# Kernel optimization log

Measured on AMD Instinct MI355X. Metric: run time of the kernel, lower is better.

Reference implementation:

```python
import jax, jax.numpy as jnp
import numpy as np

B, S, D = 4, 1024, 1024
H, HD = 16, 64  # num_heads, head_dim; H*HD == D (qkv_features)
NEG_BIG = -1e10


def setup_inputs() -> dict:
    key = jax.random.key(0)
    ks = jax.random.split(key, 16)
    inp = {
        'inputs_q': jax.random.normal(ks[0], (B, S, D), jnp.float32),
        'inputs_kv': jax.random.normal(ks[1], (B, S, D), jnp.float32),
        'pos_emb_q': jax.random.normal(ks[2], (B, S, D), jnp.float32),
        'pos_emb_k': jax.random.normal(ks[3], (B, S, D), jnp.float32),
        'pos_emb_v': jax.random.normal(ks[4], (B, S, D), jnp.float32),
        'key_padding_mask': jnp.ones((B, S), jnp.float32),
    }
    scale = 1.0 / np.sqrt(D)
    inp['wq'] = jax.random.normal(ks[5], (D, H, HD), jnp.float32) * scale
    inp['bq'] = jnp.zeros((H, HD), jnp.float32)
    inp['wk'] = jax.random.normal(ks[6], (D, H, HD), jnp.float32) * scale
    inp['bk'] = jnp.zeros((H, HD), jnp.float32)
    inp['wv'] = jax.random.normal(ks[7], (D, H, HD), jnp.float32) * scale
    inp['bv'] = jnp.zeros((H, HD), jnp.float32)
    inp['wo'] = jax.random.normal(ks[8], (H, HD, D), jnp.float32) * scale
    inp['bo'] = jnp.zeros((D,), jnp.float32)
    return inp


def reference(inputs_q, inputs_kv, pos_emb_q, pos_emb_k, pos_emb_v,
              key_padding_mask, wq, bq, wk, bk, wv, bv, wo, bo):
    # Add positional embeddings before QKV projections (DETR style).
    q_in = inputs_q + pos_emb_q
    k_in = inputs_kv + pos_emb_k
    v_in = inputs_kv + pos_emb_v
    # DenseGeneral: [b,s,f] x [f,h,d] -> [b,s,h,d]
    q = jnp.einsum('bsf,fhd->bshd', q_in, wq) + bq
    k = jnp.einsum('bsf,fhd->bshd', k_in, wk) + bk
    v = jnp.einsum('bsf,fhd->bshd', v_in, wv) + bv
    # Additive key-padding bias, broadcast to [b,1,1,kv].
    bias = ((1.0 - key_padding_mask) * NEG_BIG)[:, None, None, :]
    q = q / jnp.sqrt(jnp.asarray(HD, q.dtype))
    attn = jnp.einsum('bqhd,bkhd->bhqk', q, k) + bias
    attn = jax.nn.softmax(attn, axis=-1)
    # (train=False: no dropout; identity capture layer is a no-op.)
    x = jnp.einsum('bhqk,bkhd->bqhd', attn, v)
    # Output projection over (heads, head_dim).
    out = jnp.einsum('bqhd,hdf->bqf', x, wo) + bo
    return out
```

## Files before the change

kernel.cpp:

```cpp
#include <hip/hip_runtime.h>
#include <hip/hip_bf16.h>
#include <stdint.h>

typedef __bf16 bf16_t;
typedef __bf16 bf16x8 __attribute__((ext_vector_type(8)));
typedef __bf16 bf16x4v __attribute__((ext_vector_type(4)));
typedef float  f32x4  __attribute__((ext_vector_type(4)));
typedef float  f32x16 __attribute__((ext_vector_type(16)));
typedef unsigned int u32;
typedef u32 u32x4 __attribute__((ext_vector_type(4)));

#define NEG_BIG (-1e10f)

__device__ __forceinline__ void load_lds16(const void* gsrc, void* ldst) {
  __builtin_amdgcn_global_load_lds(
      (__attribute__((address_space(1))) void*)(gsrc),
      (__attribute__((address_space(3))) void*)(ldst), 16, 0, 0);
}

__device__ __forceinline__ u32 cvt_pk_bf16(float lo, float hi) {
  u32 r;
  asm("v_cvt_pk_bf16_f32 %0, %1, %2" : "=v"(r) : "v"(lo), "v"(hi));
  return r;
}

__global__ __launch_bounds__(256) void k_prep_w(
    const float* __restrict__ iq, const float* __restrict__ ikv,
    const float* __restrict__ pq, const float* __restrict__ pk, const float* __restrict__ pv,
    const float* __restrict__ wq, const float* __restrict__ wk,
    const float* __restrict__ wv, const float* __restrict__ wo,
    bf16_t* __restrict__ Xq, bf16_t* __restrict__ Xk, bf16_t* __restrict__ Xv,
    bf16_t* __restrict__ Wt, bf16_t* __restrict__ Wot)
{
  __shared__ float t[64][65];
  if (blockIdx.x < 4096) {
    int i = blockIdx.x * 256 + threadIdx.x;
    float4 a = ((const float4*)iq)[i], b = ((const float4*)ikv)[i];
    float4 eq = ((const float4*)pq)[i], ek = ((const float4*)pk)[i], ev = ((const float4*)pv)[i];
    bf16x4v q, k, v;
    q[0] = (bf16_t)(a.x + eq.x); q[1] = (bf16_t)(a.y + eq.y);
    q[2] = (bf16_t)(a.z + eq.z); q[3] = (bf16_t)(a.w + eq.w);
    k[0] = (bf16_t)(b.x + ek.x); k[1] = (bf16_t)(b.y + ek.y);
    k[2] = (bf16_t)(b.z + ek.z); k[3] = (bf16_t)(b.w + ek.w);
    v[0] = (bf16_t)(b.x + ev.x); v[1] = (bf16_t)(b.y + ev.y);
    v[2] = (bf16_t)(b.z + ev.z); v[3] = (bf16_t)(b.w + ev.w);
    *(bf16x4v*)&Xq[(size_t)i*4] = q;
    *(bf16x4v*)&Xk[(size_t)i*4] = k;
    *(bf16x4v*)&Xv[(size_t)i*4] = v;
  } else {
    int bid = blockIdx.x - 4096;
    int z = bid >> 8, rem = bid & 255;
    const float* src = z==0 ? wq : z==1 ? wk : z==2 ? wv : wo;
    bf16_t*      dst = z < 3 ? (Wt + (size_t)z*(1u<<20)) : Wot;
    int n0 = (rem & 15) << 6, k0 = (rem >> 4) << 6;
    int c = threadIdx.x & 63, rb = threadIdx.x >> 6;
    #pragma unroll
    for (int i = 0; i < 16; ++i) {
      int r = i*4 + rb;
      t[r][c] = src[(size_t)(k0 + r)*1024 + n0 + c];
    }
    __syncthreads();
    #pragma unroll
    for (int i = 0; i < 16; ++i) {
      int r = i*4 + rb;
      dst[(size_t)(n0 + r)*1024 + k0 + c] = (bf16_t)t[c][r];
    }
  }
}

__global__ __launch_bounds__(256, 3) void k_gemm_qkv(
    const bf16_t* __restrict__ Xq, const bf16_t* __restrict__ Xk, const bf16_t* __restrict__ Xv,
    const bf16_t* __restrict__ Wt,
    const float* __restrict__ bq, const float* __restrict__ bk, const float* __restrict__ bv,
    bf16_t* __restrict__ Qo, bf16_t* __restrict__ Ko, bf16_t* __restrict__ Vt)
{
  const int L = blockIdx.x;
  const int w = (L & 7) * 96 + (L >> 3);
  const int bx = w & 7, by = (w >> 3) & 31, bz = w >> 8;
  const int bn = bz * 8 + bx;

  const bf16_t* A = bz==0 ? Xq : bz==1 ? Xk : Xv;
  const float* bias = bz==0 ? bq : bz==1 ? bk : bv;

  __shared__ bf16_t As[128*64];
  __shared__ bf16_t Bs[128*64];

  const int tid = threadIdx.x, lane = tid & 63, wid = tid >> 6;
  const int wm = wid >> 1, wn = wid & 1;
  const int bm0 = by * 128;
  const int bn0g = bn * 128;
  const int g = lane >> 4, c = lane & 15;
  const int sr = lane >> 3, sch = lane & 7;

  f32x4 acc[4][4] = {};

  #define STAGE(kt_)                                                             \
    { _Pragma("unroll")                                                          \
      for (int i = 0; i < 4; ++i) {                                              \
        int r  = wid*32 + i*8 + sr;                                              \
        int ca = sch ^ (r & 7);                                                  \
        load_lds16(A  + (size_t)(bm0  + r)*1024 + (size_t)(kt_)*64 + ca*8,       \
                   &As[(wid*32 + i*8)*64]);                                      \
        load_lds16(Wt + (size_t)(bn0g + r)*1024 + (size_t)(kt_)*64 + ca*8,       \
                   &Bs[(wid*32 + i*8)*64]);                                      \
      } }

  for (int kt = 0; kt < 16; ++kt) {
    STAGE(kt);
    __syncthreads();
    #pragma unroll
    for (int kk = 0; kk < 2; ++kk) {
      bf16x8 af[4], bfr[4];
      #pragma unroll
      for (int m = 0; m < 4; ++m) {
        int row = wm*64 + m*16 + c;
        int ch  = (kk*4 + g) ^ (row & 7);
        af[m] = *(const bf16x8*)&As[row*64 + ch*8];
      }
      #pragma unroll
      for (int n = 0; n < 4; ++n) {
        int row = wn*64 + n*16 + c;
        int ch  = (kk*4 + g) ^ (row & 7);
        bfr[n] = *(const bf16x8*)&Bs[row*64 + ch*8];
      }
      #pragma unroll
      for (int m = 0; m < 4; ++m)
        #pragma unroll
        for (int n = 0; n < 4; ++n)
          acc[m][n] = __builtin_amdgcn_mfma_f32_16x16x32_bf16(af[m], bfr[n], acc[m][n], 0, 0, 0);
    }
    __syncthreads();
  }
  #undef STAGE

  if (bz < 2) {
    bf16_t* C = bz==0 ? Qo : Ko;
    const float scale = bz==0 ? 0.125f : 1.0f;
    #pragma unroll
    for (int n = 0; n < 4; ++n) {
      int col = (bn0g & 1023) + wn*64 + n*16 + c;
      float bn_ = bias[col];
      #pragma unroll
      for (int m = 0; m < 4; ++m) {
        int row0 = bm0 + wm*64 + m*16 + g*4;
        #pragma unroll
        for (int r = 0; r < 4; ++r)
          C[(size_t)(row0 + r)*1024 + col] = (bf16_t)((acc[m][n][r] + bn_) * scale);
      }
    }
  } else {
    #pragma unroll
    for (int n = 0; n < 4; ++n) {
      int colz = (bn0g & 1023) + wn*64 + n*16 + c;
      float bn_ = bias[colz];
      int h = colz >> 6, hd = colz & 63;
      #pragma unroll
      for (int m = 0; m < 4; ++m) {
        int row0 = bm0 + wm*64 + m*16 + g*4;
        int b = row0 >> 10, s0 = row0 & 1023;
        bf16x4v v4;
        #pragma unroll
        for (int r = 0; r < 4; ++r) v4[r] = (bf16_t)(acc[m][n][r] + bn_);
        *(bf16x4v*)&Vt[(size_t)((b*16 + h)*64 + hd)*1024 + s0] = v4;
      }
    }
  }
}

__global__ __launch_bounds__(256, 2) void k_attn2(
    const bf16_t* __restrict__ Qm, const bf16_t* __restrict__ Km,
    const bf16_t* __restrict__ Vt, const float* __restrict__ mask,
    bf16_t* __restrict__ X2)
{
  __shared__ bf16_t Ks[2][64*64];
  __shared__ bf16_t Vs[2][64*64];
  __shared__ float  bias_lds[1024];
  __shared__ float  l_lds[4][32];

  const int qt = blockIdx.x, h = blockIdx.y, b = blockIdx.z;
  const int tid = threadIdx.x, lane = tid & 63, wid = tid >> 6;
  const int lq = lane & 31;
  const int hi = lane >> 5;

  {
    float4 m4 = *(const float4*)&mask[b*1024 + tid*4];
    float4 b4;
    b4.x = (1.0f - m4.x) * NEG_BIG;
    b4.y = (1.0f - m4.y) * NEG_BIG;
    b4.z = (1.0f - m4.z) * NEG_BIG;
    b4.w = (1.0f - m4.w) * NEG_BIG;
    *(float4*)&bias_lds[tid*4] = b4;
  }

  const int q0w = qt*128 + wid*32;
  bf16x8 qf[4];
  #pragma unroll
  for (int kb = 0; kb < 4; ++kb)
    qf[kb] = *(const bf16x8*)&Qm[(size_t)(b*1024 + q0w + lq)*1024 + h*64 + kb*16 + hi*8];

  f32x16 oacc[2] = {};
  float mrow = -1e30f, lsum = 0.f;

  const int sr8 = (lane >> 3);
  const int sc8 = lane & 7;
  #define STAGE(bufi, kv0)                                                        \
    {                                                                             \
      _Pragma("unroll")                                                           \
      for (int cc = 0; cc < 2; ++cc) {                                            \
        int r  = cc*32 + wid*8 + sr8;                                             \
        int ca = sc8 ^ (r & 7);                                                   \
        load_lds16(Km + (size_t)(b*1024 + (kv0) + r)*1024 + h*64 + ca*8,          \
                   &Ks[bufi][(cc*32 + wid*8)*64]);                                \
        load_lds16(Vt + (size_t)((b*16 + h)*64 + r)*1024 + (kv0) + ca*8,          \
                   &Vs[bufi][(cc*32 + wid*8)*64]);                                \
      }                                                                           \
    }

  STAGE(0, 0);
  __syncthreads();

  for (int kt = 0; kt < 16; ++kt) {
    const int buf = kt & 1;
    if (kt < 15) STAGE(buf ^ 1, (kt + 1) * 64);

    f32x16 s[2];
    #pragma unroll
    for (int blk = 0; blk < 2; ++blk) {
      f32x16 acc = {};
      #pragma unroll
      for (int kb = 0; kb < 4; ++kb) {
        int row = blk*32 + lq;
        int ch  = (kb*2 + hi) ^ (row & 7);
        bf16x8 kf = *(const bf16x8*)&Ks[buf][row*64 + ch*8];
        acc = __builtin_amdgcn_mfma_f32_32x32x16_bf16(kf, qf[kb], acc, 0, 0, 0);
      }
      s[blk] = acc;
    }

    #pragma unroll
    for (int blk = 0; blk < 2; ++blk)
      #pragma unroll
      for (int g2 = 0; g2 < 4; ++g2) {
        float4 b4 = *(const float4*)&bias_lds[kt*64 + blk*32 + g2*8 + hi*4];
        s[blk][g2*4+0] += b4.x;
        s[blk][g2*4+1] += b4.y;
        s[blk][g2*4+2] += b4.z;
        s[blk][g2*4+3] += b4.w;
      }

    float pmax = s[0][0];
    #pragma unroll
    for (int blk = 0; blk < 2; ++blk)
      #pragma unroll
      for (int r = 0; r < 16; ++r) pmax = fmaxf(pmax, s[blk][r]);
    pmax = fmaxf(pmax, __shfl_xor(pmax, 32, 64));

    if (!__all(pmax - mrow <= 8.0f)) {
      float mnew = fmaxf(mrow, pmax);
      float sc = __expf(mrow - mnew);
      lsum *= sc;
      #pragma unroll
      for (int nb = 0; nb < 2; ++nb)
        #pragma unroll
        for (int i = 0; i < 16; ++i) oacc[nb][i] *= sc;
      mrow = mnew;
    }

    float rs = 0.f;
    #pragma unroll
    for (int blk = 0; blk < 2; ++blk)
      #pragma unroll
      for (int r = 0; r < 16; ++r) {
        float p = __expf(s[blk][r] - mrow);
        s[blk][r] = p;
        rs += p;
      }
    lsum += rs + __shfl_xor(rs, 32, 64);

    u32 paw[4][4];
    #pragma unroll
    for (int blk = 0; blk < 2; ++blk)
      #pragma unroll
      for (int half = 0; half < 2; ++half) {
        int base = half * 8;
        #pragma unroll
        for (int w2 = 0; w2 < 2; ++w2) {
          u32 x = cvt_pk_bf16(s[blk][base + 2*w2],     s[blk][base + 2*w2 + 1]);
          u32 y = cvt_pk_bf16(s[blk][base + 4 + 2*w2], s[blk][base + 4 + 2*w2 + 1]);
          asm("v_permlane32_swap_b32 %0, %1" : "+v"(x), "+v"(y));
          paw[blk*2 + half][w2]     = x;
          paw[blk*2 + half][w2 + 2] = y;
        }
      }

    #pragma unroll
    for (int ks = 0; ks < 4; ++ks) {
      u32x4 t = { paw[ks][0], paw[ks][1], paw[ks][2], paw[ks][3] };
      bf16x8 pa = __builtin_bit_cast(bf16x8, t);
      #pragma unroll
      for (int nb = 0; nb < 2; ++nb) {
        int row = nb*32 + lq;
        int ch  = (ks*2 + hi) ^ (row & 7);
        bf16x8 vf = *(const bf16x8*)&Vs[buf][row*64 + ch*8];
        oacc[nb] = __builtin_amdgcn_mfma_f32_32x32x16_bf16(pa, vf, oacc[nb], 0, 0, 0);
      }
    }
    __syncthreads();
  }

  l_lds[wid][lq] = lsum;
  __syncthreads();
  #pragma unroll
  for (int g2 = 0; g2 < 4; ++g2)
    #pragma unroll
    for (int j = 0; j < 4; ++j) {
      int reg  = g2*4 + j;
      int qrow = j + 8*g2 + 4*hi;
      float inv = 1.0f / l_lds[wid][qrow];
      #pragma unroll
      for (int nb = 0; nb < 2; ++nb)
        X2[(size_t)(b*1024 + q0w + qrow)*1024 + h*64 + nb*32 + lq] =
            (bf16_t)(oacc[nb][reg] * inv);
    }
  #undef STAGE
}

__global__ __launch_bounds__(256, 3) void k_gemm_out(
    const bf16_t* __restrict__ A, const bf16_t* __restrict__ Bt,
    const float* __restrict__ bo, float* __restrict__ C)
{
  const int L = blockIdx.x;
  const int w = (L & 7) * 32 + (L >> 3);
  const int bx = w & 7, by = w >> 3;

  __shared__ bf16_t As[128*64];
  __shared__ bf16_t Bs[128*64];

  const int tid = threadIdx.x, lane = tid & 63, wid = tid >> 6;
  const int wm = wid >> 1, wn = wid & 1;
  const int bm0 = by * 128, bn0 = bx * 128;
  const int g = lane >> 4, c = lane & 15;
  const int sr = lane >> 3, sch = lane & 7;

  f32x4 acc[4][4] = {};

  #define STAGEO(kt_)                                                            \
    { _Pragma("unroll")                                                          \
      for (int i = 0; i < 4; ++i) {                                              \
        int r  = wid*32 + i*8 + sr;                                              \
        int ca = sch ^ (r & 7);                                                  \
        load_lds16(A  + (size_t)(bm0 + r)*1024 + (size_t)(kt_)*64 + ca*8,        \
                   &As[(wid*32 + i*8)*64]);                                      \
        load_lds16(Bt + (size_t)(bn0 + r)*1024 + (size_t)(kt_)*64 + ca*8,        \
                   &Bs[(wid*32 + i*8)*64]);                                      \
      } }

  for (int kt = 0; kt < 16; ++kt) {
    STAGEO(kt);
    __syncthreads();
    #pragma unroll
    for (int kk = 0; kk < 2; ++kk) {
      bf16x8 af[4], bfr[4];
      #pragma unroll
      for (int m = 0; m < 4; ++m) {
        int row = wm*64 + m*16 + c;
        int ch  = (kk*4 + g) ^ (row & 7);
        af[m] = *(const bf16x8*)&As[row*64 + ch*8];
      }
      #pragma unroll
      for (int n = 0; n < 4; ++n) {
        int row = wn*64 + n*16 + c;
        int ch  = (kk*4 + g) ^ (row & 7);
        bfr[n] = *(const bf16x8*)&Bs[row*64 + ch*8];
      }
      #pragma unroll
      for (int m = 0; m < 4; ++m)
        #pragma unroll
        for (int n = 0; n < 4; ++n)
          acc[m][n] = __builtin_amdgcn_mfma_f32_16x16x32_bf16(af[m], bfr[n], acc[m][n], 0, 0, 0);
    }
    __syncthreads();
  }
  #undef STAGEO

  #pragma unroll
  for (int n = 0; n < 4; ++n) {
    int col = bn0 + wn*64 + n*16 + c;
    float bn_ = bo[col];
    #pragma unroll
    for (int m = 0; m < 4; ++m) {
      int row0 = bm0 + wm*64 + m*16 + g*4;
      #pragma unroll
      for (int r = 0; r < 4; ++r)
        C[(size_t)(row0 + r)*1024 + col] = acc[m][n][r] + bn_;
    }
  }
}

extern "C" void kernel_launch(void* const* d_in, const int* in_sizes, int n_in,
                              void* d_out, int out_size, void* d_ws, size_t ws_size,
                              hipStream_t stream) {
  const float* iq   = (const float*)d_in[0];
  const float* ikv  = (const float*)d_in[1];
  const float* pq   = (const float*)d_in[2];
  const float* pk   = (const float*)d_in[3];
  const float* pv   = (const float*)d_in[4];
  const float* mask = (const float*)d_in[5];
  const float* wq   = (const float*)d_in[6];
  const float* bq   = (const float*)d_in[7];
  const float* wk   = (const float*)d_in[8];
  const float* bk   = (const float*)d_in[9];
  const float* wv   = (const float*)d_in[10];
  const float* bv   = (const float*)d_in[11];
  const float* wo   = (const float*)d_in[12];
  const float* bo   = (const float*)d_in[13];
  float* out = (float*)d_out;

  char* ws = (char*)d_ws;
  bf16_t* Xq  = (bf16_t*)(ws + (size_t)( 0u<<20));
  bf16_t* Xk  = (bf16_t*)(ws + (size_t)( 8u<<20));
  bf16_t* Xv  = (bf16_t*)(ws + (size_t)(16u<<20));
  bf16_t* Wt  = (bf16_t*)(ws + (size_t)(24u<<20));
  bf16_t* Wot = (bf16_t*)(ws + (size_t)(30u<<20));
  bf16_t* Q   = (bf16_t*)(ws + (size_t)(32u<<20));
  bf16_t* K   = (bf16_t*)(ws + (size_t)(40u<<20));
  bf16_t* Vt  = (bf16_t*)(ws + (size_t)(56u<<20));
  bf16_t* X2  = (bf16_t*)(ws + (size_t)(64u<<20));

  k_prep_w<<<5120, 256, 0, stream>>>(iq, ikv, pq, pk, pv, wq, wk, wv, wo,
                                     Xq, Xk, Xv, Wt, Wot);
  k_gemm_qkv<<<768, 256, 0, stream>>>(Xq, Xk, Xv, Wt, bq, bk, bv, Q, K, Vt);
  k_attn2<<<dim3(8,16,4), 256, 0, stream>>>(Q, K, Vt, mask, X2);
  k_gemm_out<<<256, 256, 0, stream>>>(X2, Wot, bo, out);
}
```

Before: 112.1 us.

## Restructure QKV GEMM into 256x256 tiles with double-buffered phased pipeline

Rewrites the QKV projection GEMM to use 512-thread blocks that each compute a 256x256 tile, split into four 128x128 quadrant phases. Global-to-LDS loads for later k-steps are interleaved with MFMA phases, using double-buffered LDS, explicit vmcnt waits and barriers. The goal is to overlap memory traffic with compute and raise data reuse per load. It also raises wave priority around MFMA sections in both the GEMM and the attention kernel. The trade-off is much larger LDS use (128KB) and only 192 blocks, which lowers occupancy and may leave some CUs underused.

```diff
diff --git a/kernel.cpp b/kernel.cpp
--- a/kernel.cpp
+++ b/kernel.cpp
@@ -68,102 +68,128 @@
   }
 }
 
-__global__ __launch_bounds__(256, 3) void k_gemm_qkv(
+__global__ __launch_bounds__(512, 2) void k_gemm_qkv(
     const bf16_t* __restrict__ Xq, const bf16_t* __restrict__ Xk, const bf16_t* __restrict__ Xv,
     const bf16_t* __restrict__ Wt,
     const float* __restrict__ bq, const float* __restrict__ bk, const float* __restrict__ bv,
     bf16_t* __restrict__ Qo, bf16_t* __restrict__ Ko, bf16_t* __restrict__ Vt)
 {
   const int L = blockIdx.x;
-  const int w = (L & 7) * 96 + (L >> 3);
-  const int bx = w & 7, by = (w >> 3) & 31, bz = w >> 8;
-  const int bn = bz * 8 + bx;
-
+  const int w = (L & 7) * 24 + (L >> 3);
+  const int by = w & 15, bn = w >> 4;
+  const int bz = bn >> 2;
   const bf16_t* A = bz==0 ? Xq : bz==1 ? Xk : Xv;
   const float* bias = bz==0 ? bq : bz==1 ? bk : bv;
 
-  __shared__ bf16_t As[128*64];
-  __shared__ bf16_t Bs[128*64];
+  __shared__ bf16_t As[2][2][128*64];
+  __shared__ bf16_t Bs[2][2][128*64];
 
   const int tid = threadIdx.x, lane = tid & 63, wid = tid >> 6;
-  const int wm = wid >> 1, wn = wid & 1;
-  const int bm0 = by * 128;
-  const int bn0g = bn * 128;
+  const int wr = wid >> 2, wc = wid & 3;
+  const int bm0 = by * 256;
+  const int bn0g = bn * 256;
   const int g = lane >> 4, c = lane & 15;
-  const int sr = lane >> 3, sch = lane & 7;
-
-  f32x4 acc[4][4] = {};
-
-  #define STAGE(kt_)                                                             \
-    { _Pragma("unroll")                                                          \
-      for (int i = 0; i < 4; ++i) {                                              \
-        int r  = wid*32 + i*8 + sr;                                              \
-        int ca = sch ^ (r & 7);                                                  \
-        load_lds16(A  + (size_t)(bm0  + r)*1024 + (size_t)(kt_)*64 + ca*8,       \
-                   &As[(wid*32 + i*8)*64]);                                      \
-        load_lds16(Wt + (size_t)(bn0g + r)*1024 + (size_t)(kt_)*64 + ca*8,       \
-                   &Bs[(wid*32 + i*8)*64]);                                      \
-      } }
-
-  for (int kt = 0; kt < 16; ++kt) {
-    STAGE(kt);
-    __syncthreads();
-    #pragma unroll
-    for (int kk = 0; kk < 2; ++kk) {
-      bf16x8 af[4], bfr[4];
-      #pragma unroll
-      for (int m = 0; m < 4; ++m) {
-        int row = wm*64 + m*16 + c;
-        int ch  = (kk*4 + g) ^ (row & 7);
-        af[m] = *(const bf16x8*)&As[row*64 + ch*8];
-      }
-      #pragma unroll
-      for (int n = 0; n < 4; ++n) {
-        int row = wn*64 + n*16 + c;
-        int ch  = (kk*4 + g) ^ (row & 7);
-        bfr[n] = *(const bf16x8*)&Bs[row*64 + ch*8];
-      }
-      #pragma unroll
-      for (int m = 0; m < 4; ++m)
-        #pragma unroll
-        for (int n = 0; n < 4; ++n)
-          acc[m][n] = __builtin_amdgcn_mfma_f32_16x16x32_bf16(af[m], bfr[n], acc[m][n], 0, 0, 0);
-    }
-    __syncthreads();
-  }
-  #undef STAGE
-
+  const int sr = lane >> 3, sc = lane & 7;
+
+  f32x4 acc[2][2][4][2] = {};
+
+  #define STAGE_A(b, h, kt_) { _Pragma("unroll") for (int ld = 0; ld < 2; ++ld) {   \
+      int lr = ld*64 + wid*8 + sr;                                                  \
+      load_lds16(A + (size_t)(bm0 + (h)*128 + lr)*1024 + (size_t)(kt_)*64 + (sc ^ sr)*8, \
+                 &As[b][h][(ld*64 + wid*8)*64]); } }
+  #define STAGE_B(b, h, kt_) { _Pragma("unroll") for (int ld = 0; ld < 2; ++ld) {   \
+      int lr = ld*64 + wid*8 + sr;                                                  \
+      load_lds16(Wt + (size_t)(bn0g + (h)*128 + lr)*1024 + (size_t)(kt_)*64 + (sc ^ sr)*8, \
+                 &Bs[b][h][(ld*64 + wid*8)*64]); } }
+
+  #define PHASE(MH, NH, STAGE_STMT, WAIT_STMT) {                                    \
+    STAGE_STMT;                                                                     \
+    bf16x8 af[4][2], bfv[2][2];                                                     \
+    _Pragma("unroll") for (int m = 0; m < 4; ++m)                                   \
+      _Pragma("unroll") for (int kk = 0; kk < 2; ++kk)                              \
+        af[m][kk] = *(const bf16x8*)&As[buf][MH][(wr*64 + m*16 + c)*64 +            \
+                                                 (((kk)*4 + g) ^ (c & 7))*8];       \
+    _Pragma("unroll") for (int n = 0; n < 2; ++n)                                   \
+      _Pragma("unroll") for (int kk = 0; kk < 2; ++kk)                              \
+        bfv[n][kk] = *(const bf16x8*)&Bs[buf][NH][(wc*32 + n*16 + c)*64 +           \
+                                                  (((kk)*4 + g) ^ (c & 7))*8];      \
+    WAIT_STMT;                                                                      \
+    __builtin_amdgcn_sched_barrier(0);                                              \
+    __builtin_amdgcn_s_barrier();                                                   \
+    __builtin_amdgcn_sched_barrier(0);                                              \
+    __builtin_amdgcn_s_setprio(1);                                                  \
+    _Pragma("unroll") for (int m = 0; m < 4; ++m)                                   \
+      _Pragma("unroll") for (int n = 0; n < 2; ++n)                                 \
+        _Pragma("unroll") for (int kk = 0; kk < 2; ++kk)                            \
+          acc[MH][NH][m][n] = __builtin_amdgcn_mfma_f32_16x16x32_bf16(              \
+              af[m][kk], bfv[n][kk], acc[MH][NH][m][n], 0, 0, 0);                   \
+    __builtin_amdgcn_s_setprio(0);                                                  \
+    __builtin_amdgcn_sched_barrier(0);                                              \
+    __builtin_amdgcn_s_barrier();                                                   \
+    __builtin_amdgcn_sched_barrier(0);                                              \
+  }
+
+  STAGE_A(0, 0, 0); STAGE_B(0, 0, 0); STAGE_B(0, 1, 0); STAGE_A(0, 1, 0);
+  STAGE_A(1, 0, 1); STAGE_B(1, 0, 1);
+  asm volatile("s_waitcnt vmcnt(4)" ::: "memory");
+  __builtin_amdgcn_sched_barrier(0);
+  __builtin_amdgcn_s_barrier();
+  __builtin_amdgcn_sched_barrier(0);
+
+  #pragma unroll 1
+  for (int t = 0; t < 16; ++t) {
+    const int buf = t & 1;
+    PHASE(0, 0, if (t < 15) STAGE_B(buf ^ 1, 1, t + 1), );
+    PHASE(0, 1, if (t < 15) STAGE_A(buf ^ 1, 1, t + 1), );
+    PHASE(1, 0, if (t < 14) STAGE_A(buf, 0, t + 2), );
+    PHASE(1, 1, if (t < 14) STAGE_B(buf, 0, t + 2),
+          if (t < 14)       { asm volatile("s_waitcnt vmcnt(4)" ::: "memory"); }
+          else if (t == 14) { asm volatile("s_waitcnt vmcnt(0)" ::: "memory"); } );
+  }
+  #undef PHASE
+  #undef STAGE_A
+  #undef STAGE_B
+
+  const int bn0loc = (bn & 3) * 256;
   if (bz < 2) {
     bf16_t* C = bz==0 ? Qo : Ko;
     const float scale = bz==0 ? 0.125f : 1.0f;
     #pragma unroll
-    for (int n = 0; n < 4; ++n) {
-      int col = (bn0g & 1023) + wn*64 + n*16 + c;
-      float bn_ = bias[col];
-      #pragma unroll
-      for (int m = 0; m < 4; ++m) {
-        int row0 = bm0 + wm*64 + m*16 + g*4;
+    for (int mh = 0; mh < 2; ++mh)
+      #pragma unroll
+      for (int nh = 0; nh < 2; ++nh)
         #pragma unroll
-        for (int r = 0; r < 4; ++r)
-          C[(size_t)(row0 + r)*1024 + col] = (bf16_t)((acc[m][n][r] + bn_) * scale);
-      }
-    }
+        for (int n = 0; n < 2; ++n) {
+          int col = bn0loc + nh*128 + wc*32 + n*16 + c;
+          float bn_ = bias[col];
+          #pragma unroll
+          for (int m = 0; m < 4; ++m) {
+            int row0 = bm0 + mh*128 + wr*64 + m*16 + g*4;
+            #pragma unroll
+            for (int r = 0; r < 4; ++r)
+              C[(size_t)(row0 + r)*1024 + col] = (bf16_t)((acc[mh][nh][m][n][r] + bn_) * scale);
+          }
+        }
   } else {
     #pragma unroll
-    for (int n = 0; n < 4; ++n) {
-      int colz = (bn0g & 1023) + wn*64 + n*16 + c;
-      float bn_ = bias[colz];
-      int h = colz >> 6, hd = colz & 63;
-      #pragma unroll
-      for (int m = 0; m < 4; ++m) {
-        int row0 = bm0 + wm*64 + m*16 + g*4;
-        int b = row0 >> 10, s0 = row0 & 1023;
-        bf16x4v v4;
+    for (int mh = 0; mh < 2; ++mh)
+      #pragma unroll
+      for (int nh = 0; nh < 2; ++nh)
         #pragma unroll
-        for (int r = 0; r < 4; ++r) v4[r] = (bf16_t)(acc[m][n][r] + bn_);
-        *(bf16x4v*)&Vt[(size_t)((b*16 + h)*64 + hd)*1024 + s0] = v4;
-      }
-    }
+        for (int n = 0; n < 2; ++n) {
+          int colz = bn0loc + nh*128 + wc*32 + n*16 + c;
+          float bn_ = bias[colz];
+          int h = colz >> 6, hd = colz & 63;
+          #pragma unroll
+          for (int m = 0; m < 4; ++m) {
+            int row0 = bm0 + mh*128 + wr*64 + m*16 + g*4;
+            int b = row0 >> 10, s0 = row0 & 1023;
+            bf16x4v v4;
+            #pragma unroll
+            for (int r = 0; r < 4; ++r) v4[r] = (bf16_t)(acc[mh][nh][m][n][r] + bn_);
+            *(bf16x4v*)&Vt[(size_t)((b*16 + h)*64 + hd)*1024 + s0] = v4;
+          }
+        }
   }
 }
 
@@ -224,6 +250,7 @@
     if (kt < 15) STAGE(buf ^ 1, (kt + 1) * 64);
 
     f32x16 s[2];
+    __builtin_amdgcn_s_setprio(1);
     #pragma unroll
     for (int blk = 0; blk < 2; ++blk) {
       f32x16 acc = {};
@@ -236,6 +263,7 @@
       }
       s[blk] = acc;
     }
+    __builtin_amdgcn_s_setprio(0);
 
     #pragma unroll
     for (int blk = 0; blk < 2; ++blk)
@@ -293,6 +321,7 @@
         }
       }
 
+    __builtin_amdgcn_s_setprio(1);
     #pragma unroll
     for (int ks = 0; ks < 4; ++ks) {
       u32x4 t = { paw[ks][0], paw[ks][1], paw[ks][2], paw[ks][3] };
@@ -305,6 +334,7 @@
         oacc[nb] = __builtin_amdgcn_mfma_f32_32x32x16_bf16(pa, vf, oacc[nb], 0, 0, 0);
       }
     }
+    __builtin_amdgcn_s_setprio(0);
     __syncthreads();
   }
 
@@ -429,7 +459,7 @@
 
   k_prep_w<<<5120, 256, 0, stream>>>(iq, ikv, pq, pk, pv, wq, wk, wv, wo,
                                      Xq, Xk, Xv, Wt, Wot);
-  k_gemm_qkv<<<768, 256, 0, stream>>>(Xq, Xk, Xv, Wt, bq, bk, bv, Q, K, Vt);
+  k_gemm_qkv<<<192, 512, 0, stream>>>(Xq, Xk, Xv, Wt, bq, bk, bv, Q, K, Vt);
   k_attn2<<<dim3(8,16,4), 256, 0, stream>>>(Q, K, Vt, mask, X2);
   k_gemm_out<<<256, 256, 0, stream>>>(X2, Wot, bo, out);
 }
```

Measured after the change: 129.5 us. 15.5% more time.

## Load K/V fragments directly from global into registers in attention kernel

Applied to the files above, without the earlier changes.

The attention kernel no longer double-buffers K and V tiles through LDS with async global-to-LDS loads. Each wave now reads its MFMA operand fragments straight from global memory into registers, relying on L2/L1 since the four waves share the same K/V rows. This drops the per-iteration block barrier and the LDS footprint, and final normalization uses a wave shuffle instead of an LDS round trip. s_setprio is added around the MFMA sections. In exchange there is no explicit prefetch, global traffic per wave rises, and the uncoalesced strided reads may add latency.

```diff
diff --git a/kernel.cpp b/kernel.cpp
--- a/kernel.cpp
+++ b/kernel.cpp
@@ -172,10 +172,7 @@
     const bf16_t* __restrict__ Vt, const float* __restrict__ mask,
     bf16_t* __restrict__ X2)
 {
-  __shared__ bf16_t Ks[2][64*64];
-  __shared__ bf16_t Vs[2][64*64];
-  __shared__ float  bias_lds[1024];
-  __shared__ float  l_lds[4][32];
+  __shared__ float bias_lds[1024];
 
   const int qt = blockIdx.x, h = blockIdx.y, b = blockIdx.z;
   const int tid = threadIdx.x, lane = tid & 63, wid = tid >> 6;
@@ -201,47 +198,44 @@
   f32x16 oacc[2] = {};
   float mrow = -1e30f, lsum = 0.f;
 
-  const int sr8 = (lane >> 3);
-  const int sc8 = lane & 7;
-  #define STAGE(bufi, kv0)                                                        \
-    {                                                                             \
-      _Pragma("unroll")                                                           \
-      for (int cc = 0; cc < 2; ++cc) {                                            \
-        int r  = cc*32 + wid*8 + sr8;                                             \
-        int ca = sc8 ^ (r & 7);                                                   \
-        load_lds16(Km + (size_t)(b*1024 + (kv0) + r)*1024 + h*64 + ca*8,          \
-                   &Ks[bufi][(cc*32 + wid*8)*64]);                                \
-        load_lds16(Vt + (size_t)((b*16 + h)*64 + r)*1024 + (kv0) + ca*8,          \
-                   &Vs[bufi][(cc*32 + wid*8)*64]);                                \
-      }                                                                           \
-    }
-
-  STAGE(0, 0);
+  const bf16_t* Kb = Km + (size_t)(b*1024)*1024 + h*64;
+  const bf16_t* Vb = Vt + (size_t)((b*16 + h)*64)*1024;
+
   __syncthreads();
 
   for (int kt = 0; kt < 16; ++kt) {
-    const int buf = kt & 1;
-    if (kt < 15) STAGE(buf ^ 1, (kt + 1) * 64);
+    const int kv0 = kt * 64;
+
+    bf16x8 kf[2][4];
+    #pragma unroll
+    for (int blk = 0; blk < 2; ++blk)
+      #pragma unroll
+      for (int kb = 0; kb < 4; ++kb)
+        kf[blk][kb] = *(const bf16x8*)&Kb[(size_t)(kv0 + blk*32 + lq)*1024 + (kb*2 + hi)*8];
+    bf16x8 vf[4][2];
+    #pragma unroll
+    for (int ks = 0; ks < 4; ++ks)
+      #pragma unroll
+      for (int nb = 0; nb < 2; ++nb)
+        vf[ks][nb] = *(const bf16x8*)&Vb[(size_t)(nb*32 + lq)*1024 + kv0 + (ks*2 + hi)*8];
 
     f32x16 s[2];
+    __builtin_amdgcn_s_setprio(1);
     #pragma unroll
     for (int blk = 0; blk < 2; ++blk) {
       f32x16 acc = {};
       #pragma unroll
-      for (int kb = 0; kb < 4; ++kb) {
-        int row = blk*32 + lq;
-        int ch  = (kb*2 + hi) ^ (row & 7);
-        bf16x8 kf = *(const bf16x8*)&Ks[buf][row*64 + ch*8];
-        acc = __builtin_amdgcn_mfma_f32_32x32x16_bf16(kf, qf[kb], acc, 0, 0, 0);
-      }
+      for (int kb = 0; kb < 4; ++kb)
+        acc = __builtin_amdgcn_mfma_f32_32x32x16_bf16(kf[blk][kb], qf[kb], acc, 0, 0, 0);
       s[blk] = acc;
     }
+    __builtin_amdgcn_s_setprio(0);
 
     #pragma unroll
     for (int blk = 0; blk < 2; ++blk)
       #pragma unroll
       for (int g2 = 0; g2 < 4; ++g2) {
-        float4 b4 = *(const float4*)&bias_lds[kt*64 + blk*32 + g2*8 + hi*4];
+        float4 b4 = *(const float4*)&bias_lds[kv0 + blk*32 + g2*8 + hi*4];
         s[blk][g2*4+0] += b4.x;
         s[blk][g2*4+1] += b4.y;
         s[blk][g2*4+2] += b4.z;
@@ -293,36 +287,31 @@
         }
       }
 
+    __builtin_amdgcn_s_setprio(1);
     #pragma unroll
     for (int ks = 0; ks < 4; ++ks) {
       u32x4 t = { paw[ks][0], paw[ks][1], paw[ks][2], paw[ks][3] };
       bf16x8 pa = __builtin_bit_cast(bf16x8, t);
       #pragma unroll
-      for (int nb = 0; nb < 2; ++nb) {
-        int row = nb*32 + lq;
-        int ch  = (ks*2 + hi) ^ (row & 7);
-        bf16x8 vf = *(const bf16x8*)&Vs[buf][row*64 + ch*8];
-        oacc[nb] = __builtin_amdgcn_mfma_f32_32x32x16_bf16(pa, vf, oacc[nb], 0, 0, 0);
-      }
-    }
-    __syncthreads();
-  }
-
-  l_lds[wid][lq] = lsum;
-  __syncthreads();
+      for (int nb = 0; nb < 2; ++nb)
+        oacc[nb] = __builtin_amdgcn_mfma_f32_32x32x16_bf16(pa, vf[ks][nb], oacc[nb], 0, 0, 0);
+    }
+    __builtin_amdgcn_s_setprio(0);
+  }
+
+  float linv = 1.0f / lsum;
   #pragma unroll
   for (int g2 = 0; g2 < 4; ++g2)
     #pragma unroll
     for (int j = 0; j < 4; ++j) {
       int reg  = g2*4 + j;
       int qrow = j + 8*g2 + 4*hi;
-      float inv = 1.0f / l_lds[wid][qrow];
+      float inv = __shfl(linv, qrow, 64);
       #pragma unroll
       for (int nb = 0; nb < 2; ++nb)
         X2[(size_t)(b*1024 + q0w + qrow)*1024 + h*64 + nb*32 + lq] =
             (bf16_t)(oacc[nb][reg] * inv);
     }
-  #undef STAGE
 }
 
 __global__ __launch_bounds__(256, 3) void k_gemm_out(
```

After: 138.9 us. 23.9% more time.
